# Performance work log

Measured on AMD Instinct MI355X. Metric: run time of the kernel, lower is better.

## Reference

```python
import jax, jax.numpy as jnp
import numpy as np
import math

L_SIDE = 32           # one_side_length = ceil(sqrt(L)), L = 32**2
NDIM = 16             # args.ndim (SSM state size)
N_SSM = 16            # args.n_ssm
DIRS = 4              # args.directions_amount
EMBED = 1024          # embed_dim
KD = DIRS * N_SSM     # kernel_dim = 64
CDIM = EMBED * DIRS   # C_dimensions = 4096
H = EMBED // N_SSM    # 64 (channels per ssm)
R2 = 16               # expansion terms per kernel position
R = L_SIDE * L_SIDE * R2
V = 2 * L_SIDE        # vander power dim (power_dim = kernel_dim_arg*2)
BSZ = 8
SEQ = L_SIDE * L_SIDE


def _build_one_matrix():
    # Mimics CoeffCalculator.whole_as_one: for each of d=2 flow axes and each
    # of R expansion terms, the 4 A-factor rows are one-hot selectors over the
    # V power basis, and the 5th (B) row holds an integer coefficient in one of
    # the first two columns (selecting B1 or B2).
    rng = np.random.default_rng(0)
    M = np.zeros((2, 5, R, V), dtype=np.float32)
    di = np.arange(2)[:, None]
    ri = np.arange(R)[None, :]
    for a in range(4):
        idx = rng.integers(0, V, size=(2, R))
        M[di, a, ri, idx] = 1.0
    col = rng.integers(0, 2, size=(2, R))
    coef = rng.integers(1, 5, size=(2, R)).astype(np.float32)
    M[di, 4, ri, col] = coef
    return jnp.asarray(M)


def setup_inputs() -> dict:
    key = jax.random.key(0)
    ks = jax.random.split(key, 7)
    return {
        "x": jax.random.normal(ks[0], (SEQ, BSZ, EMBED), jnp.float32),
        "A": jax.random.normal(ks[1], (4, KD, NDIM), jnp.float32) * 0.2,
        "B1": jax.random.normal(ks[2], (KD, NDIM), jnp.float32) * 0.2,
        "B2": jax.random.normal(ks[3], (KD, NDIM), jnp.float32) * 0.2,
        "C1": jax.random.normal(ks[4], (CDIM, NDIM), jnp.float32),
        "C2": jax.random.normal(ks[5], (CDIM, NDIM), jnp.float32),
        "omega": jax.random.normal(ks[6], (EMBED,), jnp.float32),
        "one_matrix": _build_one_matrix(),
    }


def _compute_kernel(A, B1, B2, C1, C2, one_matrix, dtype):
    scale = 1.0 / math.sqrt(NDIM)
    # _calc_coeffs: sigmoid on A, B
    As = jax.nn.sigmoid(A)                                  # (4, KD, NDIM)
    pw = jnp.arange(V, dtype=dtype)
    # torch.linalg.vander: increasing powers 0..V-1 -> (4, V, KD, NDIM)
    A_vals = jnp.transpose(As[..., None] ** pw, (0, 3, 1, 2))
    Bs = jax.nn.sigmoid(jnp.stack([B1, B2], 0))             # (2, KD, NDIM)
    Bpad = jnp.zeros((V, KD, NDIM), dtype).at[:2].set(Bs)   # pad to V rows
    vals = jnp.concatenate([A_vals, Bpad[None]], 0)         # (5, V, KD, NDIM)
    # 'd a R V, a V k n -> d a R k n' then product over the 5 factors
    prod = jnp.einsum('drv,vkn->drkn', one_matrix[:, 0], vals[0])
    for a in range(1, 5):
        prod = prod * jnp.einsum('drv,vkn->drkn', one_matrix[:, a], vals[a])
    # sum over r2 expansion terms per kernel position
    w = prod.reshape(2, SEQ, R2, KD, NDIM).sum(2)           # (2, SEQ, KD, NDIM)
    C = jnp.stack([C1, C2], 0) * scale                      # (2, CDIM, NDIM)
    Cr = C.reshape(2, H, KD, NDIM)
    k = jnp.einsum('dpkn,dhkn->phk', w, Cr).reshape(L_SIDE, L_SIDE, CDIM)
    # boundary scaling (first row/col x2, corner net x1)
    k = k.at[0, :, :].multiply(2.0)
    k = k.at[:, 0, :].multiply(2.0)
    k = k.at[0, 0, :].divide(4.0)
    return k


def reference(x, A, B1, B2, C1, C2, omega, one_matrix):
    k = _compute_kernel(A, B1, B2, C1, C2, one_matrix, x.dtype)
    # channel layout (H, dir, n_ssm) -> per-direction (EMBED,) kernels
    kd = k.reshape(L_SIDE, L_SIDE, H, DIRS, N_SSM)
    kd = jnp.transpose(kd, (3, 2, 4, 0, 1)).reshape(DIRS, EMBED, L_SIDE, L_SIDE)
    # 4-corner scans: flip kernel per direction; conv is linear so sum kernels
    ksum = kd[0] + kd[1, :, ::-1, :] + kd[2, :, :, ::-1] + kd[3, :, ::-1, ::-1]
    residual = x * omega                                    # 'L B D, D -> L B D'
    xg = jnp.transpose(x, (1, 2, 0)).reshape(BSZ, EMBED, L_SIDE, L_SIDE)
    s = 2 * L_SIDE
    xf = jnp.fft.rfft2(xg, s=(s, s))                        # (B, D, s, s//2+1)
    kf = jnp.fft.rfft2(ksum, s=(s, s))
    y = jnp.fft.irfft2(xf * kf, s=(s, s))[..., :L_SIDE, :L_SIDE]
    y = jnp.transpose(y.reshape(BSZ, EMBED, SEQ), (2, 0, 1))  # back to (L, B, D)
    return y + residual
```

## Files before the change

### kernel.cpp

```cpp
#include <hip/hip_runtime.h>
#include <stdint.h>


typedef __attribute__((ext_vector_type(8))) short short8;
typedef __attribute__((ext_vector_type(4))) float f32x4;

__device__ inline uint16_t f2bf(float f) {
    uint32_t u = __float_as_uint(f);
    uint32_t r = (u + 0x7FFFu + ((u >> 16) & 1u)) >> 16;
    return (uint16_t)r;
}
__device__ inline float bf2f(uint16_t v) {
    return __uint_as_float((uint32_t)v << 16);
}
__device__ inline uint32_t packbf(float a, float b) {
    return (uint32_t)f2bf(a) | ((uint32_t)f2bf(b) << 16);
}

__global__ __launch_bounds__(256) void k_front(const float* __restrict__ x,
                                               uint16_t* __restrict__ xtb,
                                               const float* __restrict__ om,
                                               const float* __restrict__ A,
                                               const float* __restrict__ B1,
                                               const float* __restrict__ B2,
                                               float* __restrict__ w) {
    __shared__ __align__(16) float shf[32 * 257];
    int bx = blockIdx.x;
    int t = threadIdx.x;

    if (bx < 1024) {
        int u = bx & 31, e0 = (bx >> 5) * 32;
        {
            const float* src = x + (size_t)(u * 256 + t) * 1024 + e0;
            #pragma unroll
            for (int qq = 0; qq < 8; ++qq) {
                float4 v = *(const float4*)(src + qq * 4);
                shf[(qq * 4 + 0) * 257 + t] = v.x;
                shf[(qq * 4 + 1) * 257 + t] = v.y;
                shf[(qq * 4 + 2) * 257 + t] = v.z;
                shf[(qq * 4 + 3) * 257 + t] = v.w;
            }
        }
        __syncthreads();
        int er = t & 31, b = t >> 5;
        const float* row = shf + er * 257 + b;
        uint32_t pk[16];
        #pragma unroll
        for (int k2 = 0; k2 < 16; ++k2)
            pk[k2] = packbf(row[(2 * k2) * 8], row[(2 * k2 + 1) * 8]);
        uint16_t* dst = xtb + (size_t)(e0 + er) * 8192 + u * 256 + b * 32;
        uint4* d4 = (uint4*)dst;
        d4[0] = make_uint4(pk[0], pk[1], pk[2], pk[3]);
        d4[1] = make_uint4(pk[4], pk[5], pk[6], pk[7]);
        d4[2] = make_uint4(pk[8], pk[9], pk[10], pk[11]);
        d4[3] = make_uint4(pk[12], pk[13], pk[14], pk[15]);
    } else {
        int p = bx - 1024;
        uint32_t* sel_l = (uint32_t*)shf;
        float* coef_l = shf + 32;
        int lane = t & 63, wv = t >> 6;

        #pragma unroll
        for (int k = 0; k < 8; ++k) {
            int pi = wv * 8 + k;
            int d = pi >> 4, r2 = pi & 15;
            int r = p * 16 + r2;
            uint32_t s = 0;
            float cf = 1.0f;
            #pragma unroll
            for (int a = 0; a < 5; ++a) {
                float v = om[((size_t)(d * 5 + a) * 16384 + r) * 64 + lane];
                unsigned long long m = __ballot(v != 0.0f);
                int idx = (m != 0ull) ? __builtin_ctzll(m) : 0;
                float mv = __shfl(v, idx, 64);
                if (m == 0ull) mv = 0.0f;
                if (a < 4) {
                    s |= (uint32_t)idx << (6 * a);
                    cf *= mv;
                } else {
                    if (idx > 1) cf = 0.0f;
                    else { s |= (uint32_t)idx << 24; cf *= mv; }
                }
            }
            if (lane == 0) { sel_l[pi] = s; coef_l[pi] = cf; }
        }
        __syncthreads();

        int d = t >> 7;
        int j0 = (t & 127) * 8;
        float L0[8], L1[8], L2[8], L3[8], B0v[8], B1v[8], acc[8];
        #pragma unroll
        for (int a = 0; a < 4; ++a) {
            float* La = (a == 0) ? L0 : (a == 1) ? L1 : (a == 2) ? L2 : L3;
            float4 u0 = *(const float4*)(A + a * 1024 + j0);
            float4 u1 = *(const float4*)(A + a * 1024 + j0 + 4);
            float tmp[8] = {u0.x, u0.y, u0.z, u0.w, u1.x, u1.y, u1.z, u1.w};
            #pragma unroll
            for (int jj = 0; jj < 8; ++jj)
                La[jj] = -log2f(1.0f + expf(-tmp[jj]));
        }
        {
            float4 u0 = *(const float4*)(B1 + j0);
            float4 u1 = *(const float4*)(B1 + j0 + 4);
            float4 v0 = *(const float4*)(B2 + j0);
            float4 v1 = *(const float4*)(B2 + j0 + 4);
            float t1v[8] = {u0.x, u0.y, u0.z, u0.w, u1.x, u1.y, u1.z, u1.w};
            float t2v[8] = {v0.x, v0.y, v0.z, v0.w, v1.x, v1.y, v1.z, v1.w};
            #pragma unroll
            for (int jj = 0; jj < 8; ++jj) {
                B0v[jj] = 1.0f / (1.0f + expf(-t1v[jj]));
                B1v[jj] = 1.0f / (1.0f + expf(-t2v[jj]));
            }
        }
        #pragma unroll
        for (int jj = 0; jj < 8; ++jj) acc[jj] = 0.0f;

        #pragma unroll
        for (int r2 = 0; r2 < 16; ++r2) {
            uint32_t s = sel_l[d * 16 + r2];
            float cf = coef_l[d * 16 + r2];
            float f0 = (float)(s & 63u);
            float f1 = (float)((s >> 6) & 63u);
            float f2 = (float)((s >> 12) & 63u);
            float f3 = (float)((s >> 18) & 63u);
            int col = (int)((s >> 24) & 1u);
            float c0 = col ? 0.0f : cf;
            float c1 = col ? cf : 0.0f;
            #pragma unroll
            for (int jj = 0; jj < 8; ++jj) {
                float ex = __builtin_fmaf(f3, L3[jj],
                           __builtin_fmaf(f2, L2[jj],
                           __builtin_fmaf(f1, L1[jj], f0 * L0[jj])));
                float bs = __builtin_fmaf(c1, B1v[jj], c0 * B0v[jj]);
                acc[jj] = __builtin_fmaf(exp2f(ex), bs, acc[jj]);
            }
        }
        float* dst = w + (size_t)(d * 1024 + p) * 1024 + j0;
        *(float4*)(dst)     = make_float4(acc[0], acc[1], acc[2], acc[3]);
        *(float4*)(dst + 4) = make_float4(acc[4], acc[5], acc[6], acc[7]);
    }
}

__global__ __launch_bounds__(256) void k_kd(const float* __restrict__ w,
                                            const float* __restrict__ C1,
                                            const float* __restrict__ C2,
                                            uint16_t* __restrict__ kd4b) {
    __shared__ float Wl[128 * 33];
    __shared__ float Ctl[32 * 65];
    int kap = blockIdx.x;
    int p0 = blockIdx.y * 128;
    int dir = kap >> 4, m = kap & 15;
    int t = threadIdx.x;

    {
        int d = t >> 7, pp = t & 127;
        const float* src = w + ((size_t)(d * 1024 + p0 + pp) * 64 + kap) * 16;
        float* dst = Wl + pp * 33 + d * 16;
        #pragma unroll
        for (int q = 0; q < 4; ++q) {
            float4 v = *(const float4*)(src + q * 4);
            dst[q * 4 + 0] = v.x; dst[q * 4 + 1] = v.y;
            dst[q * 4 + 2] = v.z; dst[q * 4 + 3] = v.w;
        }
    }
    if (t < 128) {
        int d = t >> 6, h = t & 63;
        const float* Cd = d ? C2 : C1;
        const float* src = Cd + (size_t)(h * 64 + kap) * 16;
        #pragma unroll
        for (int q = 0; q < 16; ++q)
            Ctl[(d * 16 + q) * 65 + h] = src[q] * 0.25f;
    }
    __syncthreads();

    int ph = t & 15, hq = t >> 4;
    int pl = ph * 8, h0 = hq * 4;
    float acc[8][4];
    #pragma unroll
    for (int i = 0; i < 8; ++i)
        { acc[i][0] = acc[i][1] = acc[i][2] = acc[i][3] = 0.0f; }

    for (int k = 0; k < 32; ++k) {
        float c0 = Ctl[k * 65 + h0 + 0];
        float c1 = Ctl[k * 65 + h0 + 1];
        float c2 = Ctl[k * 65 + h0 + 2];
        float c3 = Ctl[k * 65 + h0 + 3];
        #pragma unroll
        for (int i = 0; i < 8; ++i) {
            float wv = Wl[(pl + i) * 33 + k];
            acc[i][0] += wv * c0; acc[i][1] += wv * c1;
            acc[i][2] += wv * c2; acc[i][3] += wv * c3;
        }
    }
    #pragma unroll
    for (int j = 0; j < 4; ++j) {
        int h = h0 + j;
        uint32_t pk[4];
        #pragma unroll
        for (int qq = 0; qq < 4; ++qq) {
            float v0, v1;
            #pragma unroll
            for (int z = 0; z < 2; ++z) {
                int p = p0 + pl + qq * 2 + z;
                int ii = p >> 5, jj = p & 31;
                float f = ((ii == 0) != (jj == 0)) ? 2.0f : 1.0f;
                float val = acc[qq * 2 + z][j] * f;
                if (z == 0) v0 = val; else v1 = val;
            }
            pk[qq] = packbf(v0, v1);
        }
        uint16_t* dst = kd4b + ((size_t)(dir * 1024 + h * 16 + m)) * 1024 + p0 + pl;
        *(uint4*)dst = make_uint4(pk[0], pk[1], pk[2], pk[3]);
    }
}

__global__ __launch_bounds__(256) void k_conv(const uint16_t* __restrict__ xtb,
                                              const uint16_t* __restrict__ kd4b,
                                              uint16_t* __restrict__ ytb) {
    __shared__ __align__(16) char smem[24576 + 16384];
    const int KROW = 768;
    const int SROW = 96;
    char* xtl = smem + 24576;

    int e = blockIdx.x;
    int t = threadIdx.x;
    int lane = t & 63, wv = t >> 6;
    int n = lane & 15, q = lane >> 4, nn = n & 7;

    {
        f32x4 z = {0.f, 0.f, 0.f, 0.f};
        #pragma unroll
        for (int k = 0; k < 6; ++k)
            *(f32x4*)(smem + (t + k * 256) * 16) = z;
    }
    {
        const uint4* src = (const uint4*)(xtb + (size_t)e * 8192);
        #pragma unroll
        for (int r = 0; r < 4; ++r) {
            uint4 v = src[r * 256 + t];
            *(uint4*)(xtl + (r * 256 + t) * 16) = v;
        }
    }
    int pi = t >> 3, pj = (t & 7) * 4;
    float s0, s1, s2, s3;
    {
        const uint16_t* b0 = kd4b + (size_t)e * 1024;
        ushort4 a0 = *(const ushort4*)(b0 + pi * 32 + pj);
        ushort4 a1 = *(const ushort4*)(b0 + (1 << 20) + (31 - pi) * 32 + pj);
        ushort4 a2 = *(const ushort4*)(b0 + (2 << 20) + pi * 32 + (28 - pj));
        ushort4 a3 = *(const ushort4*)(b0 + (3 << 20) + (31 - pi) * 32 + (28 - pj));
        s0 = bf2f(a0.x) + bf2f(a1.x) + bf2f(a2.w) + bf2f(a3.w);
        s1 = bf2f(a0.y) + bf2f(a1.y) + bf2f(a2.z) + bf2f(a3.z);
        s2 = bf2f(a0.z) + bf2f(a1.z) + bf2f(a2.y) + bf2f(a3.y);
        s3 = bf2f(a0.w) + bf2f(a1.w) + bf2f(a2.x) + bf2f(a3.x);
    }
    __syncthreads();

    {
        uint16_t k0 = f2bf(s0), k1 = f2bf(s1), k2 = f2bf(s2), k3 = f2bf(s3);
        #pragma unroll
        for (int s = 0; s < 8; ++s) {
            uint16_t* row = (uint16_t*)(smem + pi * KROW + s * SROW);
            int c = 31 + s - pj;
            row[c]     = k0;
            row[c - 1] = k1;
            row[c - 2] = k2;
            row[c - 3] = k3;
        }
    }
    __syncthreads();

    int A0 = n - 8 * q;
    int A1 = A0 + 16;
    int sh1 = (A1 + 9) & 7;
    int off1 = sh1 * SROW + (31 + sh1 - A1) * 2;
    int off0;
    if (A0 >= -8) {
        int sh0 = (A0 + 9) & 7;
        off0 = sh0 * SROW + (31 + sh0 - A0) * 2;
    } else {
        off0 = 80;
    }
    int boff = nn * 64 + q * 16;

    short8 Breg[16];
    #pragma unroll
    for (int u = 0; u < 16; ++u)
        Breg[u] = *(const short8*)(xtl + u * 512 + boff);

    f32x4 acc0[8], acc1[8];
    #pragma unroll
    for (int ii = 0; ii < 8; ++ii) {
        acc0[ii] = (f32x4){0.f, 0.f, 0.f, 0.f};
        acc1[ii] = (f32x4){0.f, 0.f, 0.f, 0.f};
    }

    #pragma unroll
    for (int dd = 0; dd < 4; ++dd) {
        if (dd <= wv) {
            const char* krow = smem + (wv - dd) * KROW;
            short8 a0 = *(const short8*)(krow + off0);
            short8 a1 = *(const short8*)(krow + off1);
            #pragma unroll
            for (int ii = 0; ii < 8; ++ii) {
                short8 bb = (ii < 4) ? Breg[dd + 4 * ii]
                                     : *(const short8*)(xtl + (dd + 4 * ii) * 512 + boff);
                acc0[ii] = __builtin_amdgcn_mfma_f32_16x16x32_bf16(a0, bb, acc0[ii], 0, 0, 0);
                acc1[ii] = __builtin_amdgcn_mfma_f32_16x16x32_bf16(a1, bb, acc1[ii], 0, 0, 0);
            }
        }
    }
    #pragma unroll
    for (int g = 1; g <= 7; ++g) {
        #pragma unroll
        for (int dd = 0; dd < 4; ++dd) {
            const char* krow = smem + (wv + 4 * g - 3 + dd) * KROW;
            short8 a0 = *(const short8*)(krow + off0);
            short8 a1 = *(const short8*)(krow + off1);
            #pragma unroll
            for (int ii = g; ii < 8; ++ii) {
                int u = 4 * (ii - g) + 3 - dd;
                short8 bb = (ii - g < 4) ? Breg[u]
                                         : *(const short8*)(xtl + u * 512 + boff);
                acc0[ii] = __builtin_amdgcn_mfma_f32_16x16x32_bf16(a0, bb, acc0[ii], 0, 0, 0);
                acc1[ii] = __builtin_amdgcn_mfma_f32_16x16x32_bf16(a1, bb, acc1[ii], 0, 0, 0);
            }
        }
    }

    if (n < 8) {
        uint16_t* base = ytb + ((size_t)(n * 1024 + e)) * 1024 + q * 4;
        #pragma unroll
        for (int ii = 0; ii < 8; ++ii) {
            int i = wv + 4 * ii;
            uint2 w0 = make_uint2(packbf(acc0[ii][0], acc0[ii][1]),
                                  packbf(acc0[ii][2], acc0[ii][3]));
            uint2 w1 = make_uint2(packbf(acc1[ii][0], acc1[ii][1]),
                                  packbf(acc1[ii][2], acc1[ii][3]));
            *(uint2*)(base + i * 32)      = w0;
            *(uint2*)(base + i * 32 + 16) = w1;
        }
    }
}

__global__ __launch_bounds__(256) void k_t2(const uint16_t* __restrict__ ytb,
                                            const float* __restrict__ x,
                                            const float* __restrict__ omega,
                                            float* __restrict__ out) {
    __shared__ float lds[32 * 129];
    int e0 = blockIdx.x * 32, p0 = blockIdx.y * 128, b = blockIdx.z;
    int t = threadIdx.x;
    {
        int er = t & 31, seg = t >> 5;
        const uint16_t* src = ytb + (size_t)(b * 1024 + e0 + er) * 1024 + p0 + seg * 16;
        uint4 v0 = *(const uint4*)src;
        uint4 v1 = *(const uint4*)(src + 8);
        float* dst = lds + er * 129 + seg * 16;
        uint32_t ww[8] = {v0.x, v0.y, v0.z, v0.w, v1.x, v1.y, v1.z, v1.w};
        #pragma unroll
        for (int k = 0; k < 8; ++k) {
            dst[2 * k]     = bf2f((uint16_t)(ww[k] & 0xFFFFu));
            dst[2 * k + 1] = bf2f((uint16_t)(ww[k] >> 16));
        }
    }
    __syncthreads();
    int pl = t >> 1, eh = (t & 1) * 16;
    int p = p0 + pl;
    const float* xs = x + ((size_t)(p * 8 + b)) * 1024 + e0 + eh;
    float* os = out + ((size_t)(p * 8 + b)) * 1024 + e0 + eh;
    #pragma unroll
    for (int qq = 0; qq < 4; ++qq) {
        float4 xv = *(const float4*)(xs + qq * 4);
        int eb = eh + qq * 4;
        float4 ov;
        ov.x = lds[(eb + 0) * 129 + pl] + xv.x * omega[e0 + eb + 0];
        ov.y = lds[(eb + 1) * 129 + pl] + xv.y * omega[e0 + eb + 1];
        ov.z = lds[(eb + 2) * 129 + pl] + xv.z * omega[e0 + eb + 2];
        ov.w = lds[(eb + 3) * 129 + pl] + xv.w * omega[e0 + eb + 3];
        *(float4*)(os + qq * 4) = ov;
    }
}

extern "C" void kernel_launch(void* const* d_in, const int* in_sizes, int n_in,
                              void* d_out, int out_size, void* d_ws, size_t ws_size,
                              hipStream_t stream) {
    (void)in_sizes; (void)n_in; (void)out_size; (void)ws_size;
    const float* x   = (const float*)d_in[0];
    const float* A   = (const float*)d_in[1];
    const float* B1  = (const float*)d_in[2];
    const float* B2  = (const float*)d_in[3];
    const float* C1  = (const float*)d_in[4];
    const float* C2  = (const float*)d_in[5];
    const float* omg = (const float*)d_in[6];
    const float* om  = (const float*)d_in[7];
    float* out = (float*)d_out;

    float* ws  = (float*)d_ws;
    uint16_t* xtb  = (uint16_t*)ws;
    uint16_t* kd4b = (uint16_t*)(ws + 4194304);
    uint16_t* ytb  = (uint16_t*)(ws + 6291456);
    float* w       = ws + 10485760;

    k_front<<<2048, 256, 0, stream>>>(x, xtb, om, A, B1, B2, w);
    k_kd   <<<dim3(64, 8), 256, 0, stream>>>(w, C1, C2, kd4b);
    k_conv <<<1024, 256, 0, stream>>>(xtb, kd4b, ytb);
    k_t2   <<<dim3(32, 8, 8), 256, 0, stream>>>(ytb, x, omg, out);
}
```

Measured before the change: 198.8 us.

## Split front kernel into preprocessing and w-expansion kernels with interleaved blocks

Splits the fused front kernel into two kernels. k_pre interleaves transpose blocks with selector-extraction blocks, reads only the two coefficient columns of the B row instead of a wave-wide ballot over it, and computes the sigmoid/log-sigmoid tables once in 6 extra blocks. k_w then builds w from the precomputed tables. The aim is to drop redundant per-block transcendental work and balance memory-heavy and compute-heavy blocks. The cost is an extra kernel launch and a global round trip for the selectors. The selector buffers alias the kd4b workspace region, which k_kd only writes after k_w has finished.

```diff
diff --git a/kernel.cpp b/kernel.cpp
--- a/kernel.cpp
+++ b/kernel.cpp
@@ -17,19 +17,23 @@
     return (uint32_t)f2bf(a) | ((uint32_t)f2bf(b) << 16);
 }
 
-__global__ __launch_bounds__(256) void k_front(const float* __restrict__ x,
-                                               uint16_t* __restrict__ xtb,
-                                               const float* __restrict__ om,
-                                               const float* __restrict__ A,
-                                               const float* __restrict__ B1,
-                                               const float* __restrict__ B2,
-                                               float* __restrict__ w) {
+__global__ __launch_bounds__(256) void k_pre(const float* __restrict__ x,
+                                             uint16_t* __restrict__ xtb,
+                                             const float* __restrict__ om,
+                                             const float* __restrict__ A,
+                                             const float* __restrict__ B1,
+                                             const float* __restrict__ B2,
+                                             uint32_t* __restrict__ selg,
+                                             float* __restrict__ coefg,
+                                             float* __restrict__ LAg,
+                                             float* __restrict__ SBg) {
     __shared__ __align__(16) float shf[32 * 257];
     int bx = blockIdx.x;
     int t = threadIdx.x;
 
-    if (bx < 1024) {
-        int u = bx & 31, e0 = (bx >> 5) * 32;
+    if (bx < 2048 && (bx & 1) == 0) {
+        int bi = bx >> 1;
+        int u = bi & 31, e0 = (bi >> 5) * 32;
         {
             const float* src = x + (size_t)(u * 256 + t) * 1024 + e0;
             #pragma unroll
@@ -54,91 +58,118 @@
         d4[1] = make_uint4(pk[4], pk[5], pk[6], pk[7]);
         d4[2] = make_uint4(pk[8], pk[9], pk[10], pk[11]);
         d4[3] = make_uint4(pk[12], pk[13], pk[14], pk[15]);
-    } else {
-        int p = bx - 1024;
-        uint32_t* sel_l = (uint32_t*)shf;
-        float* coef_l = shf + 32;
+    } else if (bx < 2048) {
+        int p = bx >> 1;
         int lane = t & 63, wv = t >> 6;
-
         #pragma unroll
         for (int k = 0; k < 8; ++k) {
             int pi = wv * 8 + k;
             int d = pi >> 4, r2 = pi & 15;
             int r = p * 16 + r2;
+            const float* rb = om + ((size_t)d * 5242880 + (size_t)r * 64);
             uint32_t s = 0;
-            float cf = 1.0f;
             #pragma unroll
-            for (int a = 0; a < 5; ++a) {
-                float v = om[((size_t)(d * 5 + a) * 16384 + r) * 64 + lane];
+            for (int a = 0; a < 4; ++a) {
+                float v = rb[(size_t)a * 1048576 + lane];
                 unsigned long long m = __ballot(v != 0.0f);
-                int idx = (m != 0ull) ? __builtin_ctzll(m) : 0;
-                float mv = __shfl(v, idx, 64);
-                if (m == 0ull) mv = 0.0f;
-                if (a < 4) {
-                    s |= (uint32_t)idx << (6 * a);
-                    cf *= mv;
-                } else {
-                    if (idx > 1) cf = 0.0f;
-                    else { s |= (uint32_t)idx << 24; cf *= mv; }
-                }
-            }
-            if (lane == 0) { sel_l[pi] = s; coef_l[pi] = cf; }
-        }
-        __syncthreads();
-
-        int d = t >> 7;
-        int j0 = (t & 127) * 8;
-        float L0[8], L1[8], L2[8], L3[8], B0v[8], B1v[8], acc[8];
-        #pragma unroll
-        for (int a = 0; a < 4; ++a) {
-            float* La = (a == 0) ? L0 : (a == 1) ? L1 : (a == 2) ? L2 : L3;
-            float4 u0 = *(const float4*)(A + a * 1024 + j0);
-            float4 u1 = *(const float4*)(A + a * 1024 + j0 + 4);
-            float tmp[8] = {u0.x, u0.y, u0.z, u0.w, u1.x, u1.y, u1.z, u1.w};
-            #pragma unroll
-            for (int jj = 0; jj < 8; ++jj)
-                La[jj] = -log2f(1.0f + expf(-tmp[jj]));
-        }
-        {
-            float4 u0 = *(const float4*)(B1 + j0);
-            float4 u1 = *(const float4*)(B1 + j0 + 4);
-            float4 v0 = *(const float4*)(B2 + j0);
-            float4 v1 = *(const float4*)(B2 + j0 + 4);
-            float t1v[8] = {u0.x, u0.y, u0.z, u0.w, u1.x, u1.y, u1.z, u1.w};
-            float t2v[8] = {v0.x, v0.y, v0.z, v0.w, v1.x, v1.y, v1.z, v1.w};
-            #pragma unroll
-            for (int jj = 0; jj < 8; ++jj) {
-                B0v[jj] = 1.0f / (1.0f + expf(-t1v[jj]));
-                B1v[jj] = 1.0f / (1.0f + expf(-t2v[jj]));
-            }
-        }
-        #pragma unroll
-        for (int jj = 0; jj < 8; ++jj) acc[jj] = 0.0f;
-
-        #pragma unroll
-        for (int r2 = 0; r2 < 16; ++r2) {
-            uint32_t s = sel_l[d * 16 + r2];
-            float cf = coef_l[d * 16 + r2];
-            float f0 = (float)(s & 63u);
-            float f1 = (float)((s >> 6) & 63u);
-            float f2 = (float)((s >> 12) & 63u);
-            float f3 = (float)((s >> 18) & 63u);
-            int col = (int)((s >> 24) & 1u);
-            float c0 = col ? 0.0f : cf;
-            float c1 = col ? cf : 0.0f;
-            #pragma unroll
-            for (int jj = 0; jj < 8; ++jj) {
-                float ex = __builtin_fmaf(f3, L3[jj],
-                           __builtin_fmaf(f2, L2[jj],
-                           __builtin_fmaf(f1, L1[jj], f0 * L0[jj])));
-                float bs = __builtin_fmaf(c1, B1v[jj], c0 * B0v[jj]);
-                acc[jj] = __builtin_fmaf(exp2f(ex), bs, acc[jj]);
-            }
-        }
-        float* dst = w + (size_t)(d * 1024 + p) * 1024 + j0;
-        *(float4*)(dst)     = make_float4(acc[0], acc[1], acc[2], acc[3]);
-        *(float4*)(dst + 4) = make_float4(acc[4], acc[5], acc[6], acc[7]);
-    }
+                uint32_t idx = ((uint32_t)__builtin_ctzll(m)) & 63u;
+                s |= idx << (6 * a);
+            }
+            if (lane == 0) {
+                float r0 = rb[4 * 1048576 + 0];
+                float r1 = rb[4 * 1048576 + 1];
+                uint32_t col = (r1 != 0.0f) ? 1u : 0u;
+                selg[d * 16384 + r] = s | (col << 24);
+                coefg[d * 16384 + r] = r0 + r1;
+            }
+        }
+    } else {
+        int i = bx - 2048;
+        int e = t * 4;
+        if (i < 4) {
+            float4 v = *(const float4*)(A + i * 1024 + e);
+            float4 o;
+            o.x = -log2f(1.0f + expf(-v.x));
+            o.y = -log2f(1.0f + expf(-v.y));
+            o.z = -log2f(1.0f + expf(-v.z));
+            o.w = -log2f(1.0f + expf(-v.w));
+            *(float4*)(LAg + i * 1024 + e) = o;
+        } else {
+            const float* Bs = (i == 4) ? B1 : B2;
+            float4 v = *(const float4*)(Bs + e);
+            float4 o;
+            o.x = 1.0f / (1.0f + expf(-v.x));
+            o.y = 1.0f / (1.0f + expf(-v.y));
+            o.z = 1.0f / (1.0f + expf(-v.z));
+            o.w = 1.0f / (1.0f + expf(-v.w));
+            *(float4*)(SBg + (i - 4) * 1024 + e) = o;
+        }
+    }
+}
+
+__global__ __launch_bounds__(256) void k_w(const uint32_t* __restrict__ selg,
+                                           const float* __restrict__ coefg,
+                                           const float* __restrict__ LAg,
+                                           const float* __restrict__ SBg,
+                                           float* __restrict__ w) {
+    __shared__ uint32_t sel_l[32];
+    __shared__ float coef_l[32];
+    int p = blockIdx.x;
+    int t = threadIdx.x;
+    if (t < 32) {
+        int d = t >> 4, r2 = t & 15;
+        sel_l[t]  = selg[d * 16384 + p * 16 + r2];
+        coef_l[t] = coefg[d * 16384 + p * 16 + r2];
+    }
+    __syncthreads();
+
+    int d = t >> 7;
+    int j0 = (t & 127) * 8;
+    float L0[8], L1[8], L2[8], L3[8], B0v[8], B1v[8], acc[8];
+    #pragma unroll
+    for (int a = 0; a < 4; ++a) {
+        float* La = (a == 0) ? L0 : (a == 1) ? L1 : (a == 2) ? L2 : L3;
+        float4 u0 = *(const float4*)(LAg + a * 1024 + j0);
+        float4 u1 = *(const float4*)(LAg + a * 1024 + j0 + 4);
+        La[0] = u0.x; La[1] = u0.y; La[2] = u0.z; La[3] = u0.w;
+        La[4] = u1.x; La[5] = u1.y; La[6] = u1.z; La[7] = u1.w;
+    }
+    {
+        float4 u0 = *(const float4*)(SBg + j0);
+        float4 u1 = *(const float4*)(SBg + j0 + 4);
+        float4 v0 = *(const float4*)(SBg + 1024 + j0);
+        float4 v1 = *(const float4*)(SBg + 1024 + j0 + 4);
+        B0v[0] = u0.x; B0v[1] = u0.y; B0v[2] = u0.z; B0v[3] = u0.w;
+        B0v[4] = u1.x; B0v[5] = u1.y; B0v[6] = u1.z; B0v[7] = u1.w;
+        B1v[0] = v0.x; B1v[1] = v0.y; B1v[2] = v0.z; B1v[3] = v0.w;
+        B1v[4] = v1.x; B1v[5] = v1.y; B1v[6] = v1.z; B1v[7] = v1.w;
+    }
+    #pragma unroll
+    for (int jj = 0; jj < 8; ++jj) acc[jj] = 0.0f;
+
+    #pragma unroll
+    for (int r2 = 0; r2 < 16; ++r2) {
+        uint32_t s = sel_l[d * 16 + r2];
+        float cf = coef_l[d * 16 + r2];
+        float f0 = (float)(s & 63u);
+        float f1 = (float)((s >> 6) & 63u);
+        float f2 = (float)((s >> 12) & 63u);
+        float f3 = (float)((s >> 18) & 63u);
+        int col = (int)((s >> 24) & 1u);
+        float c0 = col ? 0.0f : cf;
+        float c1 = col ? cf : 0.0f;
+        #pragma unroll
+        for (int jj = 0; jj < 8; ++jj) {
+            float ex = __builtin_fmaf(f3, L3[jj],
+                       __builtin_fmaf(f2, L2[jj],
+                       __builtin_fmaf(f1, L1[jj], f0 * L0[jj])));
+            float bs = __builtin_fmaf(c1, B1v[jj], c0 * B0v[jj]);
+            acc[jj] = __builtin_fmaf(exp2f(ex), bs, acc[jj]);
+        }
+    }
+    float* dst = w + (size_t)(d * 1024 + p) * 1024 + j0;
+    *(float4*)(dst)     = make_float4(acc[0], acc[1], acc[2], acc[3]);
+    *(float4*)(dst + 4) = make_float4(acc[4], acc[5], acc[6], acc[7]);
 }
 
 __global__ __launch_bounds__(256) void k_kd(const float* __restrict__ w,
@@ -400,9 +431,14 @@
     uint16_t* kd4b = (uint16_t*)(ws + 4194304);
     uint16_t* ytb  = (uint16_t*)(ws + 6291456);
     float* w       = ws + 10485760;
-
-    k_front<<<2048, 256, 0, stream>>>(x, xtb, om, A, B1, B2, w);
-    k_kd   <<<dim3(64, 8), 256, 0, stream>>>(w, C1, C2, kd4b);
-    k_conv <<<1024, 256, 0, stream>>>(xtb, kd4b, ytb);
-    k_t2   <<<dim3(32, 8, 8), 256, 0, stream>>>(ytb, x, omg, out);
-}
+    uint32_t* selg = (uint32_t*)(ws + 4194304);
+    float* coefg   = ws + 4194304 + 32768;
+    float* LAg     = ws + 4194304 + 65536;
+    float* SBg     = ws + 4194304 + 69632;
+
+    k_pre <<<2054, 256, 0, stream>>>(x, xtb, om, A, B1, B2, selg, coefg, LAg, SBg);
+    k_w   <<<1024, 256, 0, stream>>>(selg, coefg, LAg, SBg, w);
+    k_kd  <<<dim3(64, 8), 256, 0, stream>>>(w, C1, C2, kd4b);
+    k_conv<<<1024, 256, 0, stream>>>(xtb, kd4b, ytb);
+    k_t2  <<<dim3(32, 8, 8), 256, 0, stream>>>(ytb, x, omg, out);
+}
```

Measured after the change: 195.0 us. Within noise of the previous version (-1.9%).
